# Optimization experiments

Hardware: AMD Instinct MI355X
Metric: run time of the kernel (lower is better)

The kernel has to match this reference:

```python
import jax, jax.numpy as jnp
import numpy as np

GATE_THRESH = 0.4
ALPHA_FN = lambda L: 1.0 - 1.0 / L  # length-adaptive alpha, called with actual L
EPS_NORM = 1e-12  # F.normalize eps
EPS_LN = 1e-5     # LayerNorm eps


def setup_inputs() -> dict:
    key = jax.random.key(0)
    B, L, H, V = 64, 2048, 128, 32000
    ks = jax.random.split(key, 8)
    s = lambda k, shape, fan: jax.random.normal(k, shape, jnp.float32) * (1.0 / np.sqrt(fan))
    return {
        "seq": jax.random.randint(ks[0], (B, L), 0, V, dtype=jnp.int64),
        "embed_w": jax.random.normal(ks[1], (V, H), jnp.float32) * 0.02,
        "ff_w1": s(ks[2], (2 * H, H), H), "ff_b1": jnp.zeros((2 * H,), jnp.float32),
        "ff_w2": s(ks[3], (H, 2 * H), 2 * H), "ff_b2": jnp.zeros((H,), jnp.float32),
        "ln_g": jnp.ones((H,), jnp.float32), "ln_b": jnp.zeros((H,), jnp.float32),
        "kp_w": s(ks[4], (H, H), H),
        "rp_w": s(ks[5], (H, H), H), "rp_b": jnp.zeros((H,), jnp.float32),
        "out_w": s(ks[6], (V, H), H), "out_b": jnpp if False else jnp.zeros((V,), jnp.float32),
    }


def reference(seq, embed_w, ff_w1, ff_b1, ff_w2, ff_b2, ln_g, ln_b, kp_w, rp_w, rp_b, out_w, out_b):
    h = embed_w[seq]                                            # [B,L,H]
    ff = jnp.maximum(h @ ff_w1.T + ff_b1, 0.0) @ ff_w2.T + ff_b2
    x = h + ff
    mu = x.mean(-1, keepdims=True)
    var = x.var(-1, keepdims=True)                              # biased, as LayerNorm
    h = (x - mu) / jnp.sqrt(var + EPS_LN) * ln_g + ln_b
    B, L, H = h.shape
    alpha = ALPHA_FN(L)
    k_all = jnp.einsum('blh,oh->blo', h, kp_w)                  # kp has no bias

    def step(M, k):                                             # M:[B,H,H], k:[B,H]
        kn = k / jnp.maximum(jnp.linalg.norm(k, axis=-1, keepdims=True), EPS_NORM)
        vp = jnp.einsum('bij,bj->bi', M, kn)
        d = k - vp
        delta = d[:, :, None] * kn[:, None, :]                  # outer product [B,H,H]
        fire = (jnp.linalg.norm(d, axis=-1) >= GATE_THRESH * jnp.linalg.norm(k, axis=-1)).astype(k.dtype)
        return M + (1.0 - alpha) * fire[:, None, None] * delta, None

    M0 = jnp.zeros((B, H, H), h.dtype)
    M, _ = jax.lax.scan(step, M0, jnp.swapaxes(k_all[:, :-1, :], 0, 1))  # scan over L-1 steps
    q = k_all[:, -1, :]
    read = jnp.einsum('bij,bj->bi', M, q)
    return (read @ rp_w.T + rp_b) @ out_w.T + out_b             # [B,V]
```

## Files before the change

kernel.cpp:

```cpp
#include <hip/hip_runtime.h>
#include <hip/hip_bf16.h>
#include <stdint.h>

#define Bn 64
#define Ln 2048
#define Hn 128
#define Vn 32000
#define THn 256
#define LAMBDA_ (1.0f/2048.0f)
#define CC 32
#define NCH (Ln/CC)
#define KP  132
#define VS  132
#define GS  36
#define MSR 36
#define MSW 576
#define HS  132

typedef short bf16x8 __attribute__((ext_vector_type(8)));
typedef float f32x4  __attribute__((ext_vector_type(4)));

__device__ __forceinline__ float rdlane(float v, int s) {
  return __int_as_float(__builtin_amdgcn_readlane(__float_as_int(v), s));
}

template <int CTRL>
__device__ __forceinline__ float dpp_add(float x) {
  int t = __builtin_amdgcn_update_dpp(0, __float_as_int(x), CTRL, 0xf, 0xf, false);
  return x + __int_as_float(t);
}
__device__ __forceinline__ float wave_sum64(float x) {
  x = dpp_add<0x111>(x);
  x = dpp_add<0x112>(x);
  x = dpp_add<0x114>(x);
  x = dpp_add<0x118>(x);
  x = dpp_add<0x142>(x);
  x = dpp_add<0x143>(x);
  return rdlane(x, 63);
}

__device__ __forceinline__ uint32_t packhl(float x) {
  uint32_t bx = __float_as_uint(x);
  float hf = __uint_as_float(bx & 0xFFFF0000u);
  uint32_t bl = __float_as_uint(x - hf);
  return (bx >> 16) | (bl & 0xFFFF0000u);
}
__device__ __forceinline__ float unpackhl(uint32_t u) {
  return __uint_as_float(u << 16) + __uint_as_float(u & 0xFFFF0000u);
}

struct FragHL { bf16x8 h; bf16x8 l; };
__device__ __forceinline__ FragHL mkfrag(const uint32_t* u) {
  union { uint32_t a[4]; bf16x8 v; } H, L;
  H.a[0] = __builtin_amdgcn_perm(u[1], u[0], 0x05040100u);
  H.a[1] = __builtin_amdgcn_perm(u[3], u[2], 0x05040100u);
  H.a[2] = __builtin_amdgcn_perm(u[5], u[4], 0x05040100u);
  H.a[3] = __builtin_amdgcn_perm(u[7], u[6], 0x05040100u);
  L.a[0] = __builtin_amdgcn_perm(u[1], u[0], 0x07060302u);
  L.a[1] = __builtin_amdgcn_perm(u[3], u[2], 0x07060302u);
  L.a[2] = __builtin_amdgcn_perm(u[5], u[4], 0x07060302u);
  L.a[3] = __builtin_amdgcn_perm(u[7], u[6], 0x07060302u);
  FragHL f; f.h = H.v; f.l = L.v; return f;
}

__device__ __forceinline__ void ld8(const uint32_t* p, uint32_t* u) {
  const uint4 a = *reinterpret_cast<const uint4*>(p);
  const uint4 b = *reinterpret_cast<const uint4*>(p + 4);
  u[0]=a.x; u[1]=a.y; u[2]=a.z; u[3]=a.w;
  u[4]=b.x; u[5]=b.y; u[6]=b.z; u[7]=b.w;
}

__device__ __forceinline__ bf16x8 asbf(uint4 u) {
  union { uint4 a; bf16x8 v; } c; c.a = u; return c.v;
}

__device__ __forceinline__ f32x4 mfma16(bf16x8 a, bf16x8 b, f32x4 c) {
  return __builtin_amdgcn_mfma_f32_16x16x32_bf16(a, b, c, 0, 0, 0);
}

__global__ __launch_bounds__(256) void p0_pack(
    const float* __restrict__ w1, const float* __restrict__ w2,
    const float* __restrict__ kp, uint32_t* __restrict__ wp)
{
  const int id = blockIdx.x*256 + threadIdx.x;
  const float* src; uint32_t *dh, *dl; int p;
  if (id < 16384)      { src = w1; p = id;         dh = wp;         dl = wp+16384; }
  else if (id < 32768) { src = w2; p = id-16384;   dh = wp+32768;   dl = wp+49152; }
  else                 { src = kp; p = id-32768;   dh = wp+65536;   dl = wp+73728; }
  const float x0 = src[2*p], x1 = src[2*p+1];
  const uint32_t b0 = __float_as_uint(x0), b1 = __float_as_uint(x1);
  const float l0f = x0 - __uint_as_float(b0 & 0xFFFF0000u);
  const float l1f = x1 - __uint_as_float(b1 & 0xFFFF0000u);
  dh[p] = (b0 >> 16) | ((b1 >> 16) << 16);
  dl[p] = (__float_as_uint(l0f) >> 16) | ((__float_as_uint(l1f) >> 16) << 16);
}

__global__ __launch_bounds__(256, 2) void p1_fused(
    const int* __restrict__ seq,
    const float* __restrict__ embed_w,
    const uint32_t* __restrict__ wp,
    const float* __restrict__ ff_b1, const float* __restrict__ ff_b2,
    const float* __restrict__ ln_g, const float* __restrict__ ln_b,
    uint32_t* __restrict__ knp_all, float* __restrict__ norm_all)
{
  __shared__ __align__(16) uint32_t h_p[64*HS];
  __shared__ __align__(16) uint32_t u_p[64*HS];
  __shared__ float part1[256], part2[256];
  __shared__ float mul[64], rsl[64];
  __shared__ int sid[64];

  const int tid  = threadIdx.x;
  const int lane = tid & 63;
  const int w    = __builtin_amdgcn_readfirstlane(tid >> 6);
  const int q4   = lane >> 4;
  const int m16  = lane & 15;
  const int tile0 = blockIdx.x * 64;

  const uint32_t* w1h = wp;
  const uint32_t* w1l = wp + 16384;
  const uint32_t* w2h = wp + 32768;
  const uint32_t* w2l = wp + 49152;
  const uint32_t* kph = wp + 65536;
  const uint32_t* kpl = wp + 73728;

  if (tid < 64) sid[tid] = seq[tile0 + tid];
  __syncthreads();

  {
    const int t = tid >> 2, part = tid & 3;
    const float4* erow =
        reinterpret_cast<const float4*>(embed_w + (size_t)sid[t]*Hn) + part*8;
    #pragma unroll
    for (int c = 0; c < 8; ++c) {
      float4 v = erow[c];
      int j = part*32 + c*4;
      h_p[t*HS+j+0] = packhl(v.x); h_p[t*HS+j+1] = packhl(v.y);
      h_p[t*HS+j+2] = packhl(v.z); h_p[t*HS+j+3] = packhl(v.w);
    }
  }
  __syncthreads();

  f32x4 acc2[4][2];
  #pragma unroll
  for (int tt=0;tt<4;++tt)
    #pragma unroll
    for (int ct=0;ct<2;++ct) acc2[tt][ct] = (f32x4){0.f,0.f,0.f,0.f};

  #pragma unroll 1
  for (int ho=0; ho<2; ++ho) {
    #pragma unroll 1
    for (int tt=0; tt<4; ++tt) {
      FragHL fa[4];
      #pragma unroll
      for (int kk=0;kk<4;++kk) {
        uint32_t ua[8];
        ld8(&h_p[(16*tt+m16)*HS + 32*kk + 8*q4], ua);
        fa[kk] = mkfrag(ua);
      }
      #pragma unroll
      for (int ct=0; ct<2; ++ct) {
        const int ob = 128*ho + 32*w + 16*ct;
        f32x4 a = (f32x4){0.f,0.f,0.f,0.f};
        #pragma unroll
        for (int kk=0;kk<4;++kk) {
          const size_t wi = (size_t)(ob+m16)*64 + 16*kk + 4*q4;
          bf16x8 bh = asbf(*reinterpret_cast<const uint4*>(&w1h[wi]));
          bf16x8 bl = asbf(*reinterpret_cast<const uint4*>(&w1l[wi]));
          a = mfma16(fa[kk].h, bh, a);
          a = mfma16(fa[kk].h, bl, a);
          a = mfma16(fa[kk].l, bh, a);
        }
        const float bb = ff_b1[ob + m16];
        #pragma unroll
        for (int reg=0;reg<4;++reg) {
          float uv = fmaxf(a[reg] + bb, 0.f);
          u_p[(16*tt+4*q4+reg)*HS + 32*w + 16*ct + m16] = packhl(uv);
        }
      }
    }
    __syncthreads();
    #pragma unroll 1
    for (int tt=0; tt<4; ++tt) {
      FragHL fu[4];
      #pragma unroll
      for (int kk=0;kk<4;++kk) {
        uint32_t ua[8];
        ld8(&u_p[(16*tt+m16)*HS + 32*kk + 8*q4], ua);
        fu[kk] = mkfrag(ua);
      }
      #pragma unroll
      for (int ct=0; ct<2; ++ct) {
        const int ib = 32*w + 16*ct;
        f32x4 a = acc2[tt][ct];
        #pragma unroll
        for (int kk=0;kk<4;++kk) {
          const size_t wi = (size_t)(ib+m16)*128 + 64*ho + 16*kk + 4*q4;
          bf16x8 bh = asbf(*reinterpret_cast<const uint4*>(&w2h[wi]));
          bf16x8 bl = asbf(*reinterpret_cast<const uint4*>(&w2l[wi]));
          a = mfma16(fu[kk].h, bh, a);
          a = mfma16(fu[kk].h, bl, a);
          a = mfma16(fu[kk].l, bh, a);
        }
        acc2[tt][ct] = a;
      }
    }
    __syncthreads();
  }

  float xx[4][2][4];
  #pragma unroll
  for (int tt=0;tt<4;++tt)
    #pragma unroll
    for (int ct=0;ct<2;++ct) {
      const int col = 32*w + 16*ct + m16;
      const float b2 = ff_b2[col];
      #pragma unroll
      for (int reg=0;reg<4;++reg) {
        const float hval = unpackhl(h_p[(16*tt+4*q4+reg)*HS + col]);
        xx[tt][ct][reg] = acc2[tt][ct][reg] + b2 + hval;
      }
    }
  #pragma unroll
  for (int tt=0;tt<4;++tt)
    #pragma unroll
    for (int reg=0;reg<4;++reg) {
      float s1 = xx[tt][0][reg] + xx[tt][1][reg];
      float s2 = xx[tt][0][reg]*xx[tt][0][reg] + xx[tt][1][reg]*xx[tt][1][reg];
      s1 += __shfl_xor(s1,1); s1 += __shfl_xor(s1,2);
      s1 += __shfl_xor(s1,4); s1 += __shfl_xor(s1,8);
      s2 += __shfl_xor(s2,1); s2 += __shfl_xor(s2,2);
      s2 += __shfl_xor(s2,4); s2 += __shfl_xor(s2,8);
      if (m16==0) {
        part1[w*64 + 16*tt+4*q4+reg] = s1;
        part2[w*64 + 16*tt+4*q4+reg] = s2;
      }
    }
  __syncthreads();
  if (tid < 64) {
    const float mu = (part1[tid]+part1[64+tid]+part1[128+tid]+part1[192+tid])*(1.0f/128.0f);
    const float ms = (part2[tid]+part2[64+tid]+part2[128+tid]+part2[192+tid])*(1.0f/128.0f);
    mul[tid] = mu;
    rsl[tid] = rsqrtf(ms - mu*mu + 1e-5f);
  }
  __syncthreads();

  #pragma unroll
  for (int tt=0;tt<4;++tt)
    #pragma unroll
    for (int ct=0;ct<2;++ct) {
      const int col = 32*w + 16*ct + m16;
      const float g = ln_g[col], bb = ln_b[col];
      #pragma unroll
      for (int reg=0;reg<4;++reg) {
        const int tok = 16*tt+4*q4+reg;
        const float hn = (xx[tt][ct][reg] - mul[tok])*rsl[tok]*g + bb;
        h_p[tok*HS + col] = packhl(hn);
      }
    }
  __syncthreads();

  f32x4 ak[4][2];
  #pragma unroll 1
  for (int tt=0;tt<4;++tt) {
    FragHL fh[4];
    #pragma unroll
    for (int kk=0;kk<4;++kk) {
      uint32_t ua[8];
      ld8(&h_p[(16*tt+m16)*HS + 32*kk + 8*q4], ua);
      fh[kk] = mkfrag(ua);
    }
    #pragma unroll
    for (int ct=0;ct<2;++ct) {
      const int ob = 32*w + 16*ct;
      f32x4 a = (f32x4){0.f,0.f,0.f,0.f};
      #pragma unroll
      for (int kk=0;kk<4;++kk) {
        const size_t wi = (size_t)(ob+m16)*64 + 16*kk + 4*q4;
        bf16x8 bh = asbf(*reinterpret_cast<const uint4*>(&kph[wi]));
        bf16x8 bl = asbf(*reinterpret_cast<const uint4*>(&kpl[wi]));
        a = mfma16(fh[kk].h, bh, a);
        a = mfma16(fh[kk].h, bl, a);
        a = mfma16(fh[kk].l, bh, a);
      }
      ak[tt][ct] = a;
    }
  }
  #pragma unroll
  for (int tt=0;tt<4;++tt)
    #pragma unroll
    for (int reg=0;reg<4;++reg) {
      float s = ak[tt][0][reg]*ak[tt][0][reg] + ak[tt][1][reg]*ak[tt][1][reg];
      s += __shfl_xor(s,1); s += __shfl_xor(s,2);
      s += __shfl_xor(s,4); s += __shfl_xor(s,8);
      if (m16==0) part1[w*64 + 16*tt+4*q4+reg] = s;
    }
  __syncthreads();
  if (tid < 64) {
    const float nn = part1[tid]+part1[64+tid]+part1[128+tid]+part1[192+tid];
    const float nrm = sqrtf(nn);
    norm_all[tile0 + tid] = nrm;
    mul[tid] = 1.0f / fmaxf(nrm, 1e-12f);
  }
  __syncthreads();
  #pragma unroll
  for (int tt=0;tt<4;++tt)
    #pragma unroll
    for (int ct=0;ct<2;++ct) {
      const int col = 32*w + 16*ct + m16;
      #pragma unroll
      for (int reg=0;reg<4;++reg) {
        const int tok = 16*tt+4*q4+reg;
        knp_all[(size_t)(tile0+tok)*Hn + col] = packhl(ak[tt][ct][reg]*mul[tok]);
      }
    }
}

__global__ __launch_bounds__(512, 1) void p2_scan(
    const uint32_t* __restrict__ knp_all, const float* __restrict__ norm_all,
    float* __restrict__ read_ws)
{
  const int tid  = threadIdx.x;
  const int lane = tid & 63;
  const int wv   = __builtin_amdgcn_readfirstlane(tid >> 6);
  const int q    = lane >> 4;
  const int m    = lane & 15;
  const int b    = blockIdx.x;

  __shared__ __align__(16) uint32_t kn_p[2*CC*KP];
  __shared__ __align__(16) float    vp0L[CC*VS];
  __shared__ __align__(16) float    adL [CC*VS];
  __shared__ __align__(16) float    Gt  [CC*GS];
  __shared__ __align__(16) uint32_t msc [8*MSW];
  __shared__ float nrm_l[2*CC];

  f32x4 Macc[8];
  #pragma unroll
  for (int ct=0; ct<8; ++ct) Macc[ct] = (f32x4){0.f,0.f,0.f,0.f};

  const uint32_t* knb = knp_all + (size_t)b*Ln*Hn;
  const float*    nb  = norm_all + (size_t)b*Ln;

  {
    if (tid < 256) {
      const int t = tid>>3, g = tid&7;
      const uint4* src = reinterpret_cast<const uint4*>(knb + t*Hn + g*16);
      uint4* dst = reinterpret_cast<uint4*>(&kn_p[t*KP + g*16]);
      dst[0]=src[0]; dst[1]=src[1]; dst[2]=src[2]; dst[3]=src[3];
    }
    if (tid >= 256 && tid < 256+CC) nrm_l[tid-256] = nb[tid-256];
  }
  __syncthreads();

  #pragma unroll 1
  for (int ch=0; ch<NCH; ++ch) {
    const int cur = ch & 1;
    const uint32_t* knc = &kn_p[cur*CC*KP];
    const bool havenext = (ch+1 < NCH);

    uint4 pfa, pfb, pfc, pfd; float pfn = 0.f;
    if (havenext) {
      if (tid >= 64 && tid < 320) {
        const int idx = tid-64, t = idx>>3, g = idx&7;
        const uint4* src = reinterpret_cast<const uint4*>(
            knb + (size_t)(ch+1)*CC*Hn + t*Hn + g*16);
        pfa=src[0]; pfb=src[1]; pfc=src[2]; pfd=src[3];
      }
      if (tid >= 320 && tid < 320+CC) pfn = nb[(ch+1)*CC + (tid-320)];
    }

    if (wv >= 4) {
      const int ti = (wv-4)>>1, si = (wv-4)&1;
      f32x4 g4 = (f32x4){0.f,0.f,0.f,0.f};
      #pragma unroll
      for (int kk=0; kk<4; ++kk) {
        uint32_t ua[8], ub[8];
        ld8(&knc[(16*ti+m)*KP + 32*kk + 8*q], ua);
        ld8(&knc[(16*si+m)*KP + 32*kk + 8*q], ub);
        FragHL fa = mkfrag(ua), fb = mkfrag(ub);
        g4 = mfma16(fa.h, fb.h, g4);
        g4 = mfma16(fa.h, fb.l, g4);
        g4 = mfma16(fa.l, fb.h, g4);
      }
      #pragma unroll
      for (int reg=0; reg<4; ++reg)
        Gt[(16*ti + 4*q + reg)*GS + 16*si + m] = g4[reg];
    }

    {
      f32x4 v0 = (f32x4){0.f,0.f,0.f,0.f};
      f32x4 v1 = (f32x4){0.f,0.f,0.f,0.f};
      uint32_t* mybase = &msc[wv*MSW];
      #pragma unroll
      for (int kk=0; kk<4; ++kk) {
        #pragma unroll
        for (int c2=0; c2<2; ++c2) {
          const int ct = 2*kk + c2;
          #pragma unroll
          for (int reg=0; reg<4; ++reg)
            mybase[(4*q+reg)*MSR + 16*c2 + m] = packhl(Macc[ct][reg]);
        }
        uint32_t ua[8], ub[8];
        ld8(&mybase[m*MSR + 8*q], ua);
        FragHL fa = mkfrag(ua);
        ld8(&knc[m*KP + 32*kk + 8*q], ub);
        FragHL fb = mkfrag(ub);
        v0 = mfma16(fa.h, fb.h, v0);
        v0 = mfma16(fa.h, fb.l, v0);
        v0 = mfma16(fa.l, fb.h, v0);
        ld8(&knc[(16+m)*KP + 32*kk + 8*q], ub);
        fb = mkfrag(ub);
        v1 = mfma16(fa.h, fb.h, v1);
        v1 = mfma16(fa.h, fb.l, v1);
        v1 = mfma16(fa.l, fb.h, v1);
      }
      const float nr0 = nrm_l[cur*CC + m];
      const float nr1 = nrm_l[cur*CC + 16 + m];
      #pragma unroll
      for (int reg=0; reg<4; ++reg) {
        const int h = 16*wv + 4*q + reg;
        v0[reg] = nr0*unpackhl(knc[m*KP + h])      - v0[reg];
        v1[reg] = nr1*unpackhl(knc[(16+m)*KP + h]) - v1[reg];
      }
      *reinterpret_cast<f32x4*>(&vp0L[m*VS + 16*wv + 4*q]) = v0;
      *reinterpret_cast<f32x4*>(&vp0L[(16+m)*VS + 16*wv + 4*q]) = v1;
    }
    __syncthreads();

    if (wv==0) {
      float ad0[CC], ad1[CC], gr[CC];
      #pragma unroll
      for (int t=0;t<CC;++t) gr[t] = Gt[t*GS + (lane&31)];
      const float nrmv = nrm_l[cur*CC + (lane&31)];
      #pragma unroll
      for (int t=0;t<CC;++t) {
        float a0c0 = vp0L[t*VS + lane];
        float a1c0 = vp0L[t*VS + 64 + lane];
        float a0c1=0.f, a0c2=0.f, a0c3=0.f;
        float a1c1=0.f, a1c2=0.f, a1c3=0.f;
        #pragma unroll
        for (int s=0; s<t; ++s) {
          const float g = rdlane(gr[t], s);
          switch (s & 3) {
            case 0: a0c0 -= g*ad0[s]; a1c0 -= g*ad1[s]; break;
            case 1: a0c1 -= g*ad0[s]; a1c1 -= g*ad1[s]; break;
            case 2: a0c2 -= g*ad0[s]; a1c2 -= g*ad1[s]; break;
            default:a0c3 -= g*ad0[s]; a1c3 -= g*ad1[s]; break;
          }
        }
        const float acc0 = (a0c0+a0c1)+(a0c2+a0c3);
        const float acc1 = (a1c0+a1c1)+(a1c2+a1c3);
        const float sqt = wave_sum64(acc0*acc0 + acc1*acc1);
        const float nrm = rdlane(nrmv, t);
        if (ch==NCH-1 && t==CC-1) {
          const float kn0 = unpackhl(knc[t*KP + lane]);
          const float kn1 = unpackhl(knc[t*KP + 64 + lane]);
          read_ws[b*Hn + lane]      = nrm*(nrm*kn0 - acc0);
          read_ws[b*Hn + 64 + lane] = nrm*(nrm*kn1 - acc1);
        } else {
          const float at = (sqt >= 0.16f*nrm*nrm) ? LAMBDA_ : 0.f;
          ad0[t] = at*acc0; ad1[t] = at*acc1;
          adL[t*VS + lane]      = ad0[t];
          adL[t*VS + 64 + lane] = ad1[t];
        }
      }
    } else if (havenext) {
      if (tid >= 64 && tid < 320) {
        const int idx = tid-64, t = idx>>3, g = idx&7;
        uint4* dst = reinterpret_cast<uint4*>(
            &kn_p[(1-cur)*CC*KP + t*KP + g*16]);
        dst[0]=pfa; dst[1]=pfb; dst[2]=pfc; dst[3]=pfd;
      }
      if (tid >= 320 && tid < 320+CC) nrm_l[(1-cur)*CC + (tid-320)] = pfn;
    }
    __syncthreads();
    if (ch==NCH-1) break;

    {
      uint32_t ap[8];
      #pragma unroll
      for (int j=0;j<8;++j)
        ap[j] = packhl(adL[(8*q+j)*VS + 16*wv + m]);
      FragHL fa = mkfrag(ap);
      #pragma unroll
      for (int ct=0; ct<8; ++ct) {
        uint32_t bu[8];
        #pragma unroll
        for (int j=0;j<8;++j)
          bu[j] = knc[(8*q+j)*KP + 16*ct + m];
        FragHL fb = mkfrag(bu);
        Macc[ct] = mfma16(fa.h, fb.h, Macc[ct]);
        Macc[ct] = mfma16(fa.h, fb.l, Macc[ct]);
        Macc[ct] = mfma16(fa.l, fb.h, Macc[ct]);
      }
    }
  }
}

__global__ __launch_bounds__(128) void p3a(
    const float* __restrict__ read_ws, const float* __restrict__ rp_w,
    const float* __restrict__ rp_b, float* __restrict__ o1_ws)
{
  __shared__ float rd[128];
  const int b = blockIdx.x, t = threadIdx.x;
  rd[t] = read_ws[b*Hn + t];
  __syncthreads();
  float acc = rp_b[t];
  const float* wr = rp_w + t*Hn;
  #pragma unroll 4
  for (int i = 0; i < Hn; ++i) acc += rd[i]*wr[i];
  o1_ws[b*Hn + t] = acc;
}

__global__ __launch_bounds__(256) void p3b(
    const float* __restrict__ o1_ws, const float* __restrict__ out_w,
    const float* __restrict__ out_b, float* __restrict__ out)
{
  __shared__ __align__(16) float o1[8192];
  const int tid = threadIdx.x;
  #pragma unroll
  for (int c = 0; c < 32; ++c) o1[c*256+tid] = o1_ws[c*256+tid];
  __syncthreads();
  const int v = blockIdx.x*256 + tid;
  float acc[64];
  const float ob = out_b[v];
  #pragma unroll
  for (int bb = 0; bb < 64; ++bb) acc[bb] = ob;
  const float4* wrow = reinterpret_cast<const float4*>(out_w + (size_t)v*Hn);
  #pragma unroll 1
  for (int r4 = 0; r4 < 32; ++r4) {
    const float4 wv = wrow[r4];
    #pragma unroll
    for (int bb = 0; bb < 64; ++bb) {
      const float4 ov = *reinterpret_cast<const float4*>(&o1[bb*Hn + r4*4]);
      acc[bb] += wv.x*ov.x + wv.y*ov.y + wv.z*ov.z + wv.w*ov.w;
    }
  }
  #pragma unroll
  for (int bb = 0; bb < 64; ++bb) out[(size_t)bb*Vn + v] = acc[bb];
}

extern "C" void kernel_launch(void* const* d_in, const int* in_sizes, int n_in,
                              void* d_out, int out_size, void* d_ws, size_t ws_size,
                              hipStream_t stream)
{
  const int*   seq     = (const int*)  d_in[0];
  const float* embed_w = (const float*)d_in[1];
  const float* ff_w1   = (const float*)d_in[2];
  const float* ff_b1   = (const float*)d_in[3];
  const float* ff_w2   = (const float*)d_in[4];
  const float* ff_b2   = (const float*)d_in[5];
  const float* ln_g    = (const float*)d_in[6];
  const float* ln_b    = (const float*)d_in[7];
  const float* kp_w    = (const float*)d_in[8];
  const float* rp_w    = (const float*)d_in[9];
  const float* rp_b    = (const float*)d_in[10];
  const float* out_w   = (const float*)d_in[11];
  const float* out_b   = (const float*)d_in[12];

  float* ws          = (float*)d_ws;
  uint32_t* knp_all  = (uint32_t*)ws;
  float* norm_all    = ws + (size_t)Bn*Ln*Hn;
  float* read_ws     = norm_all + (size_t)Bn*Ln;
  float* o1_ws       = read_ws + Bn*Hn;
  uint32_t* wp       = (uint32_t*)(o1_ws + Bn*Hn);

  p0_pack<<<dim3(160), dim3(256), 0, stream>>>(ff_w1, ff_w2, kp_w, wp);
  p1_fused<<<dim3(2048), dim3(256), 0, stream>>>(
      seq, embed_w, wp, ff_b1, ff_b2, ln_g, ln_b, knp_all, norm_all);
  p2_scan<<<dim3(64), dim3(512), 0, stream>>>(knp_all, norm_all, read_ws);
  p3a<<<dim3(64), dim3(128), 0, stream>>>(read_ws, rp_w, rp_b, o1_ws);
  p3b<<<dim3(125), dim3(256), 0, stream>>>(o1_ws, out_w, out_b, (float*)d_out);
}
```

Measured before the change: 759.1 us.

## Overlap next-chunk M·k and Gram computation with serial gated scan in p2_scan

Restructures the chunked delta-rule scan so a dedicated wave (wave 0) runs the serial gated recurrence while eight other waves compute the next chunk's M·k projection and Gram matrices from the pre-update M. The missing contribution of the current chunk's updates is applied afterwards as a small correction matmul (ad × cross-Gram GxT). To make this possible, the block grows to 576 threads, k buffers become triple-buffered with a two-chunk-ahead prefetch, and the Gram matrix is double-buffered. The intent is to take the per-chunk vp computation off the serial critical path, at the cost of extra MFMA work, more LDS, and the added correction step.

```diff
diff --git a/kernel.cpp b/kernel.cpp
--- a/kernel.cpp
+++ b/kernel.cpp
@@ -12,7 +12,9 @@
 #define NCH (Ln/CC)
 #define KP  132
 #define VS  132
+#define ADS 131
 #define GS  36
+#define GXS 33
 #define MSR 36
 #define MSW 576
 #define HS  132
@@ -315,7 +317,7 @@
     }
 }
 
-__global__ __launch_bounds__(512, 1) void p2_scan(
+__global__ __launch_bounds__(576, 1) void p2_scan(
     const uint32_t* __restrict__ knp_all, const float* __restrict__ norm_all,
     float* __restrict__ read_ws)
 {
@@ -326,12 +328,13 @@
   const int m    = lane & 15;
   const int b    = blockIdx.x;
 
-  __shared__ __align__(16) uint32_t kn_p[2*CC*KP];
+  __shared__ __align__(16) uint32_t kn_p[3*CC*KP];
   __shared__ __align__(16) float    vp0L[CC*VS];
-  __shared__ __align__(16) float    adL [CC*VS];
-  __shared__ __align__(16) float    Gt  [CC*GS];
+  __shared__ __align__(16) float    adL [CC*ADS+4];
+  __shared__ __align__(16) float    Gt  [2*CC*GS];
+  __shared__ __align__(16) float    GxT [CC*GXS];
   __shared__ __align__(16) uint32_t msc [8*MSW];
-  __shared__ float nrm_l[2*CC];
+  __shared__ float nrm_l[3*CC];
 
   f32x4 Macc[8];
   #pragma unroll
@@ -346,36 +349,26 @@
       const uint4* src = reinterpret_cast<const uint4*>(knb + t*Hn + g*16);
       uint4* dst = reinterpret_cast<uint4*>(&kn_p[t*KP + g*16]);
       dst[0]=src[0]; dst[1]=src[1]; dst[2]=src[2]; dst[3]=src[3];
-    }
-    if (tid >= 256 && tid < 256+CC) nrm_l[tid-256] = nb[tid-256];
-  }
-  __syncthreads();
-
-  #pragma unroll 1
-  for (int ch=0; ch<NCH; ++ch) {
-    const int cur = ch & 1;
-    const uint32_t* knc = &kn_p[cur*CC*KP];
-    const bool havenext = (ch+1 < NCH);
-
-    uint4 pfa, pfb, pfc, pfd; float pfn = 0.f;
-    if (havenext) {
-      if (tid >= 64 && tid < 320) {
-        const int idx = tid-64, t = idx>>3, g = idx&7;
-        const uint4* src = reinterpret_cast<const uint4*>(
-            knb + (size_t)(ch+1)*CC*Hn + t*Hn + g*16);
-        pfa=src[0]; pfb=src[1]; pfc=src[2]; pfd=src[3];
-      }
-      if (tid >= 320 && tid < 320+CC) pfn = nb[(ch+1)*CC + (tid-320)];
-    }
-
-    if (wv >= 4) {
-      const int ti = (wv-4)>>1, si = (wv-4)&1;
+    } else if (tid < 512) {
+      const int idx = tid-256, t = idx>>3, g = idx&7;
+      const uint4* src = reinterpret_cast<const uint4*>(knb + CC*Hn + t*Hn + g*16);
+      uint4* dst = reinterpret_cast<uint4*>(&kn_p[CC*KP + t*KP + g*16]);
+      dst[0]=src[0]; dst[1]=src[1]; dst[2]=src[2]; dst[3]=src[3];
+    } else {
+      nrm_l[tid-512] = nb[tid-512];
+    }
+  }
+  __syncthreads();
+
+  {
+    if (wv >= 5) {
+      const int ti = (wv-5)>>1, si = (wv-5)&1;
       f32x4 g4 = (f32x4){0.f,0.f,0.f,0.f};
       #pragma unroll
       for (int kk=0; kk<4; ++kk) {
         uint32_t ua[8], ub[8];
-        ld8(&knc[(16*ti+m)*KP + 32*kk + 8*q], ua);
-        ld8(&knc[(16*si+m)*KP + 32*kk + 8*q], ub);
+        ld8(&kn_p[(16*ti+m)*KP + 32*kk + 8*q], ua);
+        ld8(&kn_p[(16*si+m)*KP + 32*kk + 8*q], ub);
         FragHL fa = mkfrag(ua), fb = mkfrag(ub);
         g4 = mfma16(fa.h, fb.h, g4);
         g4 = mfma16(fa.h, fb.l, g4);
@@ -385,51 +378,50 @@
       for (int reg=0; reg<4; ++reg)
         Gt[(16*ti + 4*q + reg)*GS + 16*si + m] = g4[reg];
     }
-
-    {
-      f32x4 v0 = (f32x4){0.f,0.f,0.f,0.f};
-      f32x4 v1 = (f32x4){0.f,0.f,0.f,0.f};
-      uint32_t* mybase = &msc[wv*MSW];
-      #pragma unroll
-      for (int kk=0; kk<4; ++kk) {
-        #pragma unroll
-        for (int c2=0; c2<2; ++c2) {
-          const int ct = 2*kk + c2;
-          #pragma unroll
-          for (int reg=0; reg<4; ++reg)
-            mybase[(4*q+reg)*MSR + 16*c2 + m] = packhl(Macc[ct][reg]);
-        }
-        uint32_t ua[8], ub[8];
-        ld8(&mybase[m*MSR + 8*q], ua);
-        FragHL fa = mkfrag(ua);
-        ld8(&knc[m*KP + 32*kk + 8*q], ub);
-        FragHL fb = mkfrag(ub);
-        v0 = mfma16(fa.h, fb.h, v0);
-        v0 = mfma16(fa.h, fb.l, v0);
-        v0 = mfma16(fa.l, fb.h, v0);
-        ld8(&knc[(16+m)*KP + 32*kk + 8*q], ub);
-        fb = mkfrag(ub);
-        v1 = mfma16(fa.h, fb.h, v1);
-        v1 = mfma16(fa.h, fb.l, v1);
-        v1 = mfma16(fa.l, fb.h, v1);
-      }
-      const float nr0 = nrm_l[cur*CC + m];
-      const float nr1 = nrm_l[cur*CC + 16 + m];
+    if (wv >= 1) {
+      const int h0 = 16*(wv-1);
+      const float nr0 = nrm_l[m], nr1 = nrm_l[16+m];
+      const uint4 r0 = *reinterpret_cast<const uint4*>(&kn_p[m*KP + h0 + 4*q]);
+      const uint4 r1 = *reinterpret_cast<const uint4*>(&kn_p[(16+m)*KP + h0 + 4*q]);
+      const uint32_t* pr0 = &r0.x; const uint32_t* pr1 = &r1.x;
       #pragma unroll
       for (int reg=0; reg<4; ++reg) {
-        const int h = 16*wv + 4*q + reg;
-        v0[reg] = nr0*unpackhl(knc[m*KP + h])      - v0[reg];
-        v1[reg] = nr1*unpackhl(knc[(16+m)*KP + h]) - v1[reg];
-      }
-      *reinterpret_cast<f32x4*>(&vp0L[m*VS + 16*wv + 4*q]) = v0;
-      *reinterpret_cast<f32x4*>(&vp0L[(16+m)*VS + 16*wv + 4*q]) = v1;
-    }
-    __syncthreads();
+        const int h = h0 + 4*q + reg;
+        vp0L[m*VS + h]      = nr0*unpackhl(pr0[reg]);
+        vp0L[(16+m)*VS + h] = nr1*unpackhl(pr1[reg]);
+      }
+    }
+  }
+  __syncthreads();
+
+  #pragma unroll 1
+  for (int ch=0; ch<NCH; ++ch) {
+    const int cur = ch%3, nx1 = (ch+1)%3, nx2 = (ch+2)%3;
+    const int sel = ch & 1;
+    const uint32_t* knc = &kn_p[cur*CC*KP];
+    const uint32_t* knN = &kn_p[nx1*CC*KP];
+    const bool havn  = (ch+1 < NCH);
+    const bool havn2 = (ch+2 < NCH);
+
+    uint4 pfa, pfb, pfc, pfd; float pfn = 0.f;
+    if (havn2) {
+      if (tid >= 320) {
+        const int idx = tid-320, t = idx>>3, g = idx&7;
+        const uint4* src = reinterpret_cast<const uint4*>(
+            knb + (size_t)(ch+2)*CC*Hn + t*Hn + g*16);
+        pfa=src[0]; pfb=src[1]; pfc=src[2]; pfd=src[3];
+      }
+      if (tid >= 288 && tid < 320) pfn = nb[(ch+2)*CC + (tid-288)];
+    }
+
+    f32x4 v0 = (f32x4){0.f,0.f,0.f,0.f};
+    f32x4 v1 = (f32x4){0.f,0.f,0.f,0.f};
 
     if (wv==0) {
       float ad0[CC], ad1[CC], gr[CC];
-      #pragma unroll
-      for (int t=0;t<CC;++t) gr[t] = Gt[t*GS + (lane&31)];
+      const float* GtS = &Gt[sel*CC*GS];
+      #pragma unroll
+      for (int t=0;t<CC;++t) gr[t] = GtS[t*GS + (lane&31)];
       const float nrmv = nrm_l[cur*CC + (lane&31)];
       #pragma unroll
       for (int t=0;t<CC;++t) {
@@ -459,40 +451,144 @@
         } else {
           const float at = (sqt >= 0.16f*nrm*nrm) ? LAMBDA_ : 0.f;
           ad0[t] = at*acc0; ad1[t] = at*acc1;
-          adL[t*VS + lane]      = ad0[t];
-          adL[t*VS + 64 + lane] = ad1[t];
-        }
-      }
-    } else if (havenext) {
-      if (tid >= 64 && tid < 320) {
-        const int idx = tid-64, t = idx>>3, g = idx&7;
-        uint4* dst = reinterpret_cast<uint4*>(
-            &kn_p[(1-cur)*CC*KP + t*KP + g*16]);
-        dst[0]=pfa; dst[1]=pfb; dst[2]=pfc; dst[3]=pfd;
-      }
-      if (tid >= 320 && tid < 320+CC) nrm_l[(1-cur)*CC + (tid-320)] = pfn;
+          adL[t*ADS + lane]      = ad0[t];
+          adL[t*ADS + 64 + lane] = ad1[t];
+        }
+      }
+    } else {
+      if (havn) {
+        uint32_t* mybase = &msc[(wv-1)*MSW];
+        #pragma unroll
+        for (int kk=0; kk<4; ++kk) {
+          #pragma unroll
+          for (int c2=0; c2<2; ++c2) {
+            const int ct = 2*kk + c2;
+            #pragma unroll
+            for (int reg=0; reg<4; ++reg)
+              mybase[(4*q+reg)*MSR + 16*c2 + m] = packhl(Macc[ct][reg]);
+          }
+          uint32_t ua[8], ub[8];
+          ld8(&mybase[m*MSR + 8*q], ua);
+          FragHL fa = mkfrag(ua);
+          ld8(&knN[m*KP + 32*kk + 8*q], ub);
+          FragHL fb = mkfrag(ub);
+          v0 = mfma16(fa.h, fb.h, v0);
+          v0 = mfma16(fa.h, fb.l, v0);
+          v0 = mfma16(fa.l, fb.h, v0);
+          ld8(&knN[(16+m)*KP + 32*kk + 8*q], ub);
+          fb = mkfrag(ub);
+          v1 = mfma16(fa.h, fb.h, v1);
+          v1 = mfma16(fa.h, fb.l, v1);
+          v1 = mfma16(fa.l, fb.h, v1);
+        }
+        if (wv <= 4) {
+          const int tj = (wv-1)>>1, ts = (wv-1)&1;
+          f32x4 g4 = (f32x4){0.f,0.f,0.f,0.f};
+          #pragma unroll
+          for (int kk=0; kk<4; ++kk) {
+            uint32_t ua[8], ub[8];
+            ld8(&knN[(16*tj+m)*KP + 32*kk + 8*q], ua);
+            ld8(&knc[(16*ts+m)*KP + 32*kk + 8*q], ub);
+            FragHL fa = mkfrag(ua), fb = mkfrag(ub);
+            g4 = mfma16(fa.h, fb.h, g4);
+            g4 = mfma16(fa.h, fb.l, g4);
+            g4 = mfma16(fa.l, fb.h, g4);
+          }
+          #pragma unroll
+          for (int reg=0; reg<4; ++reg)
+            GxT[(16*tj + 4*q + reg)*GXS + 16*ts + m] = g4[reg];
+        } else {
+          const int ti = (wv-5)>>1, si = (wv-5)&1;
+          f32x4 g4 = (f32x4){0.f,0.f,0.f,0.f};
+          #pragma unroll
+          for (int kk=0; kk<4; ++kk) {
+            uint32_t ua[8], ub[8];
+            ld8(&knN[(16*ti+m)*KP + 32*kk + 8*q], ua);
+            ld8(&knN[(16*si+m)*KP + 32*kk + 8*q], ub);
+            FragHL fa = mkfrag(ua), fb = mkfrag(ub);
+            g4 = mfma16(fa.h, fb.h, g4);
+            g4 = mfma16(fa.h, fb.l, g4);
+            g4 = mfma16(fa.l, fb.h, g4);
+          }
+          #pragma unroll
+          for (int reg=0; reg<4; ++reg)
+            Gt[(1-sel)*CC*GS + (16*ti + 4*q + reg)*GS + 16*si + m] = g4[reg];
+        }
+      }
+      if (havn2) {
+        if (tid >= 320) {
+          const int idx = tid-320, t = idx>>3, g = idx&7;
+          uint4* dst = reinterpret_cast<uint4*>(
+              &kn_p[nx2*CC*KP + t*KP + g*16]);
+          dst[0]=pfa; dst[1]=pfb; dst[2]=pfc; dst[3]=pfd;
+        }
+        if (tid >= 288 && tid < 320) nrm_l[nx2*CC + (tid-288)] = pfn;
+      }
     }
     __syncthreads();
     if (ch==NCH-1) break;
 
-    {
-      uint32_t ap[8];
-      #pragma unroll
-      for (int j=0;j<8;++j)
-        ap[j] = packhl(adL[(8*q+j)*VS + 16*wv + m]);
-      FragHL fa = mkfrag(ap);
-      #pragma unroll
-      for (int ct=0; ct<8; ++ct) {
-        uint32_t bu[8];
+    if (wv >= 1) {
+      const int h0 = 16*(wv-1);
+      {
+        uint32_t ap[8];
         #pragma unroll
         for (int j=0;j<8;++j)
-          bu[j] = knc[(8*q+j)*KP + 16*ct + m];
-        FragHL fb = mkfrag(bu);
-        Macc[ct] = mfma16(fa.h, fb.h, Macc[ct]);
-        Macc[ct] = mfma16(fa.h, fb.l, Macc[ct]);
-        Macc[ct] = mfma16(fa.l, fb.h, Macc[ct]);
-      }
-    }
+          ap[j] = packhl(adL[(8*q+j)*ADS + h0 + m]);
+        FragHL fa = mkfrag(ap);
+        #pragma unroll
+        for (int ct=0; ct<8; ++ct) {
+          uint32_t bu[8];
+          #pragma unroll
+          for (int j=0;j<8;++j)
+            bu[j] = knc[(8*q+j)*KP + 16*ct + m];
+          FragHL fb = mkfrag(bu);
+          Macc[ct] = mfma16(fa.h, fb.h, Macc[ct]);
+          Macc[ct] = mfma16(fa.h, fb.l, Macc[ct]);
+          Macc[ct] = mfma16(fa.l, fb.h, Macc[ct]);
+        }
+      }
+      f32x4 c0 = (f32x4){0.f,0.f,0.f,0.f};
+      f32x4 c1 = (f32x4){0.f,0.f,0.f,0.f};
+      {
+        uint32_t* mybase = &msc[(wv-1)*MSW];
+        #pragma unroll
+        for (int c2=0; c2<2; ++c2)
+          #pragma unroll
+          for (int reg=0; reg<4; ++reg)
+            mybase[(4*q+reg)*MSR + 16*c2 + m] =
+                packhl(adL[(16*c2+m)*ADS + h0 + 4*q + reg]);
+        uint32_t ua[8], gb[8];
+        ld8(&mybase[m*MSR + 8*q], ua);
+        FragHL fa = mkfrag(ua);
+        #pragma unroll
+        for (int jj=0;jj<8;++jj) gb[jj] = packhl(GxT[m*GXS + 8*q + jj]);
+        FragHL fb = mkfrag(gb);
+        c0 = mfma16(fa.h, fb.h, c0);
+        c0 = mfma16(fa.h, fb.l, c0);
+        c0 = mfma16(fa.l, fb.h, c0);
+        #pragma unroll
+        for (int jj=0;jj<8;++jj) gb[jj] = packhl(GxT[(16+m)*GXS + 8*q + jj]);
+        fb = mkfrag(gb);
+        c1 = mfma16(fa.h, fb.h, c1);
+        c1 = mfma16(fa.h, fb.l, c1);
+        c1 = mfma16(fa.l, fb.h, c1);
+      }
+      {
+        const float nr0 = nrm_l[nx1*CC + m];
+        const float nr1 = nrm_l[nx1*CC + 16 + m];
+        const uint4 r0 = *reinterpret_cast<const uint4*>(&knN[m*KP + h0 + 4*q]);
+        const uint4 r1 = *reinterpret_cast<const uint4*>(&knN[(16+m)*KP + h0 + 4*q]);
+        const uint32_t* pr0 = &r0.x; const uint32_t* pr1 = &r1.x;
+        #pragma unroll
+        for (int reg=0; reg<4; ++reg) {
+          const int h = h0 + 4*q + reg;
+          vp0L[m*VS + h]      = nr0*unpackhl(pr0[reg]) - v0[reg] - c0[reg];
+          vp0L[(16+m)*VS + h] = nr1*unpackhl(pr1[reg]) - v1[reg] - c1[reg];
+        }
+      }
+    }
+    __syncthreads();
   }
 }
 
@@ -567,7 +663,7 @@
   p0_pack<<<dim3(160), dim3(256), 0, stream>>>(ff_w1, ff_w2, kp_w, wp);
   p1_fused<<<dim3(2048), dim3(256), 0, stream>>>(
       seq, embed_w, wp, ff_b1, ff_b2, ln_g, ln_b, knp_all, norm_all);
-  p2_scan<<<dim3(64), dim3(512), 0, stream>>>(knp_all, norm_all, read_ws);
+  p2_scan<<<dim3(64), dim3(576), 0, stream>>>(knp_all, norm_all, read_ws);
   p3a<<<dim3(64), dim3(128), 0, stream>>>(read_ws, rp_w, rp_b, o1_ws);
   p3b<<<dim3(125), dim3(256), 0, stream>>>(o1_ws, out_w, out_b, (float*)d_out);
 }
```

After: 721.8 us. -4.9%, faster.
